# Optimization experiments

Measured on AMD Instinct MI355X. Metric: run time of the kernel, lower is better.

The kernel has to match this reference:

```python
import jax, jax.numpy as jnp
import numpy as np
import math

EMB_DIM = 1024
N_HEADS = 16
HEAD_DIM = EMB_DIM // N_HEADS
B, T = 4, 2048


def bitlinear(x, w):
    # BitNet b1.58 absmean ternary quantization. NOTE: the source never
    # rescales the ternary weights by `scale`, so forward uses raw {-1,0,1}.
    scale = jnp.maximum(jnp.mean(jnp.abs(w)), 1e-8)
    w_ternary = jnp.clip(jnp.round(w / scale), -1.0, 1.0)
    w_q = w + jax.lax.stop_gradient(w_ternary - w)  # STE
    return x @ w_q.T


def setup_inputs() -> dict:
    key = jax.random.key(0)
    k1, k2, k3 = jax.random.split(key, 3)
    x = jax.random.normal(k1, (B, T, EMB_DIM), dtype=jnp.float32)
    w_qkv = jax.random.normal(k2, (3 * EMB_DIM, EMB_DIM), dtype=jnp.float32) * 0.02
    w_out = jax.random.normal(k3, (EMB_DIM, EMB_DIM), dtype=jnp.float32) * 0.02
    return {"x": x, "w_qkv": w_qkv, "w_out": w_out}


def reference(x, w_qkv, w_out):
    Bc, Tc, C = x.shape
    qkv = bitlinear(x, w_qkv)  # [B, T, 3C]
    q, k, v = jnp.split(qkv, 3, axis=2)

    def split_heads(t):  # [B, T, C] -> [B, H, T, D]
        return t.reshape(Bc, Tc, N_HEADS, HEAD_DIM).transpose(0, 2, 1, 3)

    q, k, v = split_heads(q), split_heads(k), split_heads(v)
    scale = math.sqrt(HEAD_DIM)
    scores = jnp.einsum("bhqd,bhkd->bhqk", q, k) / scale  # [B, H, T, T]
    causal = jnp.triu(jnp.ones((Tc, Tc), dtype=bool), k=1)
    scores = jnp.where(causal, -jnp.inf, scores)
    attn = jax.nn.softmax(scores, axis=-1)
    out = jnp.einsum("bhqk,bhkd->bhqd", attn, v)  # [B, H, T, D]
    out = out.transpose(0, 2, 1, 3).reshape(Bc, Tc, C)
    return bitlinear(out, w_out)
```

## Files before the change

kernel.cpp:

```cpp
#include <hip/hip_runtime.h>
#include <hip/hip_bf16.h>

#define EMB   1024
#define NHEAD 16
#define HDIM  64
#define BSZ   4
#define SEQ   2048
#define MROWS (BSZ*SEQ)
#define NQKV  (3*EMB)

typedef __bf16 bf16;
typedef __bf16 bf16v4 __attribute__((ext_vector_type(4)));
typedef __bf16 bf16v8 __attribute__((ext_vector_type(8)));
typedef float  f32v4  __attribute__((ext_vector_type(4)));
typedef float  f32v16 __attribute__((ext_vector_type(16)));
typedef int    i32v4  __attribute__((ext_vector_type(4)));
typedef int    i32v16 __attribute__((ext_vector_type(16)));

#define MFMA16(a,b,c)   __builtin_amdgcn_mfma_f32_16x16x32_bf16((a),(b),(c),0,0,0)
#define MFMA32B(a,b,c)  __builtin_amdgcn_mfma_f32_32x32x16_bf16((a),(b),(c),0,0,0)
#define MFMAI8_32(a,b,c) __builtin_amdgcn_mfma_i32_32x32x32_i8((a),(b),(c),0,0,0)

__device__ __forceinline__ void gload_lds16(const void* g, void* l) {
  __builtin_amdgcn_global_load_lds((const __attribute__((address_space(1))) void*)g,
                                   (__attribute__((address_space(3))) void*)l,
                                   16, 0, 0);
}

#define DPP_FMAX(x, ctrl) do {                                                     \
    int _t = __builtin_amdgcn_update_dpp(0, __float_as_int(x), (ctrl), 0xf, 0xf, true); \
    (x) = fmaxf((x), __int_as_float(_t)); } while (0)


__global__ void abs_sum_kernel(const float* __restrict__ w, int n, float* out) {
  float s = 0.f;
  for (int i = blockIdx.x * blockDim.x + threadIdx.x; i < n; i += gridDim.x * blockDim.x)
    s += fabsf(w[i]);
  #pragma unroll
  for (int off = 32; off; off >>= 1) s += __shfl_down(s, off, 64);
  __shared__ float red[4];
  int lane = threadIdx.x & 63, wid = threadIdx.x >> 6;
  if (lane == 0) red[wid] = s;
  __syncthreads();
  if (threadIdx.x == 0) atomicAdd(out, red[0] + red[1] + red[2] + red[3]);
}

__global__ void ternarize_both_kernel(const float* __restrict__ wqkv,
                                      const float* __restrict__ wout,
                                      const float* __restrict__ sums,
                                      char* __restrict__ out8,
                                      bf16* __restrict__ outb) {
  int i = blockIdx.x * blockDim.x + threadIdx.x;
  const int N1 = NQKV * EMB;
  if (i < N1) {
    float scale = fmaxf(sums[0] / (float)N1, 1e-8f);
    float t = rintf(wqkv[i] / scale);
    out8[i] = (char)(int)fmaxf(-1.f, fminf(1.f, t));
  } else {
    int j = i - N1;
    float scale = fmaxf(sums[1] / (float)(EMB * EMB), 1e-8f);
    float t = rintf(wout[j] / scale);
    outb[j] = (bf16)fmaxf(-1.f, fminf(1.f, t));
  }
}

__global__ void quant_x_kernel(const float* __restrict__ x, char* __restrict__ p1,
                               char* __restrict__ p2, int n) {
  int i = blockIdx.x * blockDim.x + threadIdx.x;
  if (i >= n) return;
  float v = x[i];
  float q1 = fminf(fmaxf(rintf(v * 16.f), -127.f), 127.f);
  float r = v - q1 * 0.0625f;
  float q2 = fminf(fmaxf(rintf(r * 4096.f), -127.f), 127.f);
  p1[i] = (char)(int)q1;
  p2[i] = (char)(int)q2;
}


__launch_bounds__(256, 2)
__global__ void gemm_qkv_kernel(const char* __restrict__ xq1, const char* __restrict__ xq2,
                                const char* __restrict__ w8,
                                bf16* __restrict__ qh, bf16* __restrict__ ql,
                                bf16* __restrict__ kh, bf16* __restrict__ kl,
                                bf16* __restrict__ vt) {
  __shared__ __align__(16) char A1[3][128 * 64];
  __shared__ __align__(16) char A2[3][128 * 64];
  __shared__ __align__(16) char Bs[3][128 * 64];
  const int tid = threadIdx.x;
  const int lane = tid & 63, wid = tid >> 6;
  const int c31 = lane & 31, half = lane >> 5;
  const int m0 = blockIdx.x * 128, n0 = blockIdx.y * 128;
  const int wm = (wid >> 1) * 64, wn = (wid & 1) * 64;
  i32v16 acc1[2][2] = {};
  i32v16 acc2[2][2] = {};

  auto stage = [&](int bi, int kt) {
    #pragma unroll
    for (int r = 0; r < 2; ++r) {
      int li = r * 256 + tid;
      int row = li >> 2, cs = li & 3;
      int cg = cs ^ ((row >> 1) & 3);
      gload_lds16(xq1 + (size_t)(m0 + row) * EMB + kt * 64 + cg * 16, &A1[bi][li * 16]);
      gload_lds16(xq2 + (size_t)(m0 + row) * EMB + kt * 64 + cg * 16, &A2[bi][li * 16]);
      gload_lds16(w8  + (size_t)(n0 + row) * EMB + kt * 64 + cg * 16, &Bs[bi][li * 16]);
    }
  };

  stage(0, 0);
  for (int kt = 0; kt < EMB / 64; ++kt) {
    const int bi = kt % 3;
    if (kt + 1 < EMB / 64) {
      stage((kt + 1) % 3, kt + 1);
      asm volatile("s_waitcnt vmcnt(6)" ::: "memory");
    } else {
      asm volatile("s_waitcnt vmcnt(0)" ::: "memory");
    }
    __builtin_amdgcn_s_barrier();
    i32v4 a1[2][2], a2[2][2], bq[2][2];
    #pragma unroll
    for (int ks = 0; ks < 2; ++ks)
      #pragma unroll
      for (int tt = 0; tt < 2; ++tt) {
        int arow = wm + tt * 32 + c31;
        int aslot = (ks * 2 + half) ^ ((arow >> 1) & 3);
        a1[ks][tt] = *(const i32v4*)&A1[bi][arow * 64 + aslot * 16];
        a2[ks][tt] = *(const i32v4*)&A2[bi][arow * 64 + aslot * 16];
        int brow = wn + tt * 32 + c31;
        int bslot = (ks * 2 + half) ^ ((brow >> 1) & 3);
        bq[ks][tt] = *(const i32v4*)&Bs[bi][brow * 64 + bslot * 16];
      }
    #pragma unroll
    for (int ks = 0; ks < 2; ++ks)
      #pragma unroll
      for (int ti = 0; ti < 2; ++ti)
        #pragma unroll
        for (int tj = 0; tj < 2; ++tj) {
          acc1[ti][tj] = MFMAI8_32(a1[ks][ti], bq[ks][tj], acc1[ti][tj]);
          acc2[ti][tj] = MFMAI8_32(a2[ks][ti], bq[ks][tj], acc2[ti][tj]);
        }
  }
  const float S1 = 0.0625f, S2 = 1.f / 4096.f;
  const float QSCALE = 0.18033688011112042f;
  #pragma unroll
  for (int ti = 0; ti < 2; ++ti)
    #pragma unroll
    for (int tj = 0; tj < 2; ++tj) {
      const int n = n0 + wn + tj * 32 + c31;
      const int region = n >> 10, c1 = n & 1023, h = c1 >> 6, d = c1 & 63;
      #pragma unroll
      for (int g = 0; g < 4; ++g) {
        const int m_b = m0 + wm + ti * 32 + 8 * g + 4 * half;
        float c[4];
        #pragma unroll
        for (int rr = 0; rr < 4; ++rr)
          c[rr] = (float)acc1[ti][tj][g * 4 + rr] * S1 + (float)acc2[ti][tj][g * 4 + rr] * S2;
        if (region == 0) {
          #pragma unroll
          for (int rr = 0; rr < 4; ++rr) {
            int m = m_b + rr;
            int b = m >> 11, t = m & (SEQ - 1);
            size_t idx = (((size_t)(b * NHEAD + h) * SEQ + t) << 6) + d;
            float cs = c[rr] * QSCALE;
            bf16 hi = (bf16)cs;
            qh[idx] = hi; ql[idx] = (bf16)(cs - (float)hi);
          }
        } else if (region == 1) {
          #pragma unroll
          for (int rr = 0; rr < 4; ++rr) {
            int m = m_b + rr;
            int b = m >> 11, t = m & (SEQ - 1);
            size_t idx = (((size_t)(b * NHEAD + h) * SEQ + t) << 6) + d;
            bf16 hi = (bf16)c[rr];
            kh[idx] = hi; kl[idx] = (bf16)(c[rr] - (float)hi);
          }
        } else {
          bf16v4 pk;
          #pragma unroll
          for (int rr = 0; rr < 4; ++rr) pk[rr] = (bf16)c[rr];
          int b = m_b >> 11, t = m_b & (SEQ - 1);
          *(bf16v4*)&vt[((size_t)(b * NHEAD + h) * HDIM + d) * SEQ + t] = pk;
        }
      }
    }
}


__launch_bounds__(256, 2)
__global__ void attn_kernel(const bf16* __restrict__ qh, const bf16* __restrict__ ql,
                            const bf16* __restrict__ kh, const bf16* __restrict__ kl,
                            const bf16* __restrict__ vt, bf16* __restrict__ o) {
  __shared__ __align__(16) char smem[66560];
  bf16* Qh = (bf16*)smem;
  bf16* Ql = (bf16*)(smem + 16384);
  bf16* Pw = (bf16*)(smem + 49152);
  const int tid = threadIdx.x;
  const int lane = tid & 63, wid = tid >> 6;
  const int quad = lane >> 4, l16 = lane & 15;
  const int xs = l16 & 7;
  const int pair = blockIdx.x;
  const int bh = blockIdx.y;
  const size_t base = (size_t)bh * SEQ * HDIM;

  auto stage_kv = [&](char* dst, int k0) {
    #pragma unroll
    for (int r = 0; r < 2; ++r) {
      int li = r * 256 + tid;
      int srow = li >> 3, scg = (li & 7) ^ (srow & 7);
      gload_lds16(kh + base + (size_t)(k0 + srow) * HDIM + scg * 8, (bf16*)dst + (size_t)li * 8);
      gload_lds16(kl + base + (size_t)(k0 + srow) * HDIM + scg * 8, (bf16*)(dst + 8192) + (size_t)li * 8);
      gload_lds16(vt + base + (size_t)srow * SEQ + k0 + scg * 8,    (bf16*)(dst + 16384) + (size_t)li * 8);
    }
  };

  bf16v8 ones_f;
  {
    bf16 v1 = (l16 == 0) ? (bf16)1.0f : (bf16)0.0f;
    #pragma unroll
    for (int j = 0; j < 8; ++j) ones_f[j] = v1;
  }
  const int b = bh >> 4, h = bh & 15;

  for (int phase = 0; phase < 2; ++phase) {
    const int qt = phase ? (7 - pair) : (8 + pair);
    const int q0 = qt * 128;

    __syncthreads();
    #pragma unroll
    for (int r = 0; r < 4; ++r) {
      int li = r * 256 + tid;
      int row = li >> 3, cg = (li & 7) ^ (row & 7);
      gload_lds16(qh + base + (size_t)(q0 + row) * HDIM + cg * 8, &Qh[li * 8]);
      gload_lds16(ql + base + (size_t)(q0 + row) * HDIM + cg * 8, &Ql[li * 8]);
    }
    __syncthreads();
    bf16v8 qhf[2][2], qlf[2][2];
    #pragma unroll
    for (int sub = 0; sub < 2; ++sub)
      #pragma unroll
      for (int kk = 0; kk < 2; ++kk) {
        int off = (wid * 32 + sub * 16 + l16) * 64 + (((kk << 2) | quad) ^ xs) * 8;
        qhf[sub][kk] = *(const bf16v8*)&Qh[off];
        qlf[sub][kk] = *(const bf16v8*)&Ql[off];
      }
    __syncthreads();

    f32v4 oacc[2][4] = {};
    f32v4 lacc[2] = {};
    float mrow[2][4];
    #pragma unroll
    for (int s = 0; s < 2; ++s)
      #pragma unroll
      for (int r = 0; r < 4; ++r) mrow[s][r] = -1e30f;

    const int qw0 = q0 + wid * 32;
    const int qrow_hi = qw0 + 31;
    const int ntiles = 2 * qt + 2;

    stage_kv(smem, 0);

    for (int ktile = 0; ktile < ntiles; ++ktile) {
      char* cb = smem + (size_t)((ktile & 1) * 24576);
      char* nb = smem + (size_t)(((ktile + 1) & 1) * 24576);
      __syncthreads();
      if (ktile + 1 < ntiles) stage_kv(nb, (ktile + 1) * 64);
      const int k0 = ktile * 64;
      if (k0 > qrow_hi) continue;

      bf16* Kh_ = (bf16*)cb;
      bf16* Kl_ = (bf16*)(cb + 8192);
      bf16* Vt_ = (bf16*)(cb + 16384);

      f32v4 sacc[2][4] = {};
      #pragma unroll
      for (int kk = 0; kk < 2; ++kk) {
        const int co = (((kk << 2) | quad) ^ xs) * 8;
        bf16v8 khf[4], klf[4];
        #pragma unroll
        for (int nt = 0; nt < 4; ++nt) {
          khf[nt] = *(const bf16v8*)&Kh_[(nt * 16 + l16) * 64 + co];
          klf[nt] = *(const bf16v8*)&Kl_[(nt * 16 + l16) * 64 + co];
        }
        #pragma unroll
        for (int sub = 0; sub < 2; ++sub)
          #pragma unroll
          for (int nt = 0; nt < 4; ++nt) {
            sacc[sub][nt] = MFMA16(qhf[sub][kk], khf[nt], sacc[sub][nt]);
            sacc[sub][nt] = MFMA16(qhf[sub][kk], klf[nt], sacc[sub][nt]);
            sacc[sub][nt] = MFMA16(qlf[sub][kk], khf[nt], sacc[sub][nt]);
          }
      }

      #pragma unroll
      for (int sub = 0; sub < 2; ++sub) {
        if (k0 > qw0 + sub * 16 + 15) continue;
        const int qrow_base = qw0 + sub * 16 + quad * 4;
        #pragma unroll
        for (int nt = 0; nt < 4; ++nt) {
          int key = k0 + nt * 16 + l16;
          #pragma unroll
          for (int r = 0; r < 4; ++r)
            if (key > qrow_base + r) sacc[sub][nt][r] = -1e30f;
        }
        float alpha[4];
        #pragma unroll
        for (int r = 0; r < 4; ++r) {
          float mx = fmaxf(fmaxf(sacc[sub][0][r], sacc[sub][1][r]),
                           fmaxf(sacc[sub][2][r], sacc[sub][3][r]));
          DPP_FMAX(mx, 0x128);
          DPP_FMAX(mx, 0x124);
          DPP_FMAX(mx, 0x122);
          DPP_FMAX(mx, 0x121);
          float mnew = fmaxf(mrow[sub][r], mx);
          alpha[r] = __builtin_amdgcn_exp2f(mrow[sub][r] - mnew);
          mrow[sub][r] = mnew;
        }
        bf16* pwave = Pw + (wid * 2 + sub) * (16 * 68);
        #pragma unroll
        for (int nt = 0; nt < 4; ++nt)
          #pragma unroll
          for (int r = 0; r < 4; ++r)
            pwave[(quad * 4 + r) * 68 + nt * 16 + l16] =
                (bf16)__builtin_amdgcn_exp2f(sacc[sub][nt][r] - mrow[sub][r]);
        #pragma unroll
        for (int r = 0; r < 4; ++r) {
          lacc[sub][r] *= alpha[r];
          #pragma unroll
          for (int dt = 0; dt < 4; ++dt) oacc[sub][dt][r] *= alpha[r];
        }
      }

      #pragma unroll
      for (int kk = 0; kk < 2; ++kk) {
        const int co = (((kk << 2) | quad) ^ xs) * 8;
        bf16v8 vf[4];
        #pragma unroll
        for (int dt = 0; dt < 4; ++dt)
          vf[dt] = *(const bf16v8*)&Vt_[(dt * 16 + l16) * 64 + co];
        #pragma unroll
        for (int sub = 0; sub < 2; ++sub) {
          if (k0 > qw0 + sub * 16 + 15) continue;
          bf16v8 pf = *(const bf16v8*)&Pw[(wid * 2 + sub) * (16 * 68) + l16 * 68 + kk * 32 + quad * 8];
          lacc[sub] = MFMA16(pf, ones_f, lacc[sub]);
          #pragma unroll
          for (int dt = 0; dt < 4; ++dt)
            oacc[sub][dt] = MFMA16(pf, vf[dt], oacc[sub][dt]);
        }
      }
    }

    #pragma unroll
    for (int sub = 0; sub < 2; ++sub) {
      float lrow[4];
      #pragma unroll
      for (int r = 0; r < 4; ++r) lrow[r] = __shfl(lacc[sub][r], lane & 48, 64);
      #pragma unroll
      for (int dt = 0; dt < 4; ++dt)
        #pragma unroll
        for (int r = 0; r < 4; ++r) {
          int q = q0 + wid * 32 + sub * 16 + quad * 4 + r;
          int d = dt * 16 + l16;
          float val = oacc[sub][dt][r] / lrow[r];
          o[((size_t)(b * SEQ + q)) * EMB + h * HDIM + d] = (bf16)val;
        }
    }
  }
}


__launch_bounds__(256, 2)
__global__ void gemm_out_kernel(const bf16* __restrict__ oin, const bf16* __restrict__ wt,
                                float* __restrict__ out) {
  __shared__ __align__(16) bf16 As_[128 * 64];
  __shared__ __align__(16) bf16 Bs_[128 * 64];
  const int tid = threadIdx.x;
  const int lane = tid & 63, wid = tid >> 6;
  const int c31 = lane & 31, half = lane >> 5;
  const int m0 = blockIdx.x * 128, n0 = blockIdx.y * 128;
  const int wm = (wid >> 1) * 64, wn = (wid & 1) * 64;
  f32v16 acc[2][2] = {};

  for (int kt = 0; kt < EMB / 64; ++kt) {
    __syncthreads();
    #pragma unroll
    for (int r = 0; r < 4; ++r) {
      int li = r * 256 + tid;
      int row = li >> 3, cs = li & 7;
      int cg = cs ^ (row & 7);
      gload_lds16(oin + (size_t)(m0 + row) * EMB + kt * 64 + cg * 8, &As_[li * 8]);
      gload_lds16(wt  + (size_t)(n0 + row) * EMB + kt * 64 + cg * 8, &Bs_[li * 8]);
    }
    __syncthreads();
    bf16v8 af[4][2], bq[4][2];
    #pragma unroll
    for (int ks = 0; ks < 4; ++ks)
      #pragma unroll
      for (int tt = 0; tt < 2; ++tt) {
        int arow = wm + tt * 32 + c31;
        int aslot = (2 * ks + half) ^ (arow & 7);
        af[ks][tt] = *(const bf16v8*)&As_[arow * 64 + aslot * 8];
        int brow = wn + tt * 32 + c31;
        int bslot = (2 * ks + half) ^ (brow & 7);
        bq[ks][tt] = *(const bf16v8*)&Bs_[brow * 64 + bslot * 8];
      }
    #pragma unroll
    for (int ks = 0; ks < 4; ++ks)
      #pragma unroll
      for (int ti = 0; ti < 2; ++ti)
        #pragma unroll
        for (int tj = 0; tj < 2; ++tj)
          acc[ti][tj] = MFMA32B(af[ks][ti], bq[ks][tj], acc[ti][tj]);
  }
  #pragma unroll
  for (int ti = 0; ti < 2; ++ti)
    #pragma unroll
    for (int tj = 0; tj < 2; ++tj) {
      const int n = n0 + wn + tj * 32 + c31;
      #pragma unroll
      for (int g = 0; g < 4; ++g) {
        const int m_b = m0 + wm + ti * 32 + 8 * g + 4 * half;
        #pragma unroll
        for (int rr = 0; rr < 4; ++rr)
          out[(size_t)(m_b + rr) * EMB + n] = acc[ti][tj][g * 4 + rr];
      }
    }
}


extern "C" void kernel_launch(void* const* d_in, const int* in_sizes, int n_in,
                              void* d_out, int out_size, void* d_ws, size_t ws_size,
                              hipStream_t stream) {
  const float* x     = (const float*)d_in[0];
  const float* w_qkv = (const float*)d_in[1];
  const float* w_out = (const float*)d_in[2];
  float* out = (float*)d_out;
  char* ws = (char*)d_ws;

  const size_t SZ  = (size_t)MROWS * EMB * sizeof(bf16);
  const size_t SZ8 = (size_t)MROWS * EMB;
  size_t off = 0;
  float* sums = (float*)ws;            off = 256;
  char*  wq8  = (char*)(ws + off);     off += (size_t)NQKV * EMB;
  bf16*  wo_t = (bf16*)(ws + off);     off += (size_t)EMB * EMB * sizeof(bf16);
  char*  xq1  = (char*)(ws + off);     off += SZ8;
  char*  xq2  = (char*)(ws + off);     off += SZ8;
  bf16*  qh   = (bf16*)(ws + off);     off += SZ;
  bf16*  ql   = (bf16*)(ws + off);     off += SZ;
  bf16*  kh   = (bf16*)(ws + off);     off += SZ;
  bf16*  kl   = (bf16*)(ws + off);     off += SZ;
  bf16*  vt   = (bf16*)(ws + off);     off += SZ;
  bf16*  ob   = (bf16*)xq1;
  (void)in_sizes; (void)n_in; (void)out_size; (void)ws_size;

  hipMemsetAsync(sums, 0, 2 * sizeof(float), stream);
  abs_sum_kernel<<<256, 256, 0, stream>>>(w_qkv, NQKV * EMB, &sums[0]);
  abs_sum_kernel<<<256, 256, 0, stream>>>(w_out, EMB * EMB, &sums[1]);
  ternarize_both_kernel<<<(NQKV * EMB + EMB * EMB) / 256, 256, 0, stream>>>(w_qkv, w_out, sums, wq8, wo_t);
  quant_x_kernel<<<(MROWS * EMB) / 256, 256, 0, stream>>>(x, xq1, xq2, MROWS * EMB);
  gemm_qkv_kernel<<<dim3(MROWS / 128, NQKV / 128), 256, 0, stream>>>(xq1, xq2, wq8, qh, ql, kh, kl, vt);
  attn_kernel<<<dim3(8, BSZ * NHEAD), 256, 0, stream>>>(qh, ql, kh, kl, vt, ob);
  gemm_out_kernel<<<dim3(MROWS / 128, EMB / 128), 256, 0, stream>>>(ob, wo_t, out);
}
```

Measured before the change: 326.9 us.

## Vectorize prep kernels, add MFMA priority hints, multi-buffer output GEMM

The abs-sum, ternarize and activation-quantize kernels now load float4 and store 4-wide vectors, which cuts instruction count and memory transactions in these bandwidth-bound passes. The attention kernel wraps its MFMA sections in s_setprio so matrix work is issued ahead of other waves. The output GEMM moves from a single-buffered 64-wide K tile with two barriers per step to a 4-slot ring of 32-wide tiles, prefetching two tiles ahead with explicit vmcnt waits and one barrier per step, so global loads overlap compute. The hand-counted vmcnt values and the new swizzle must match exactly, or the GEMM reads stale or wrong data.

```diff
diff --git a/kernel.cpp b/kernel.cpp
--- a/kernel.cpp
+++ b/kernel.cpp
@@ -16,6 +16,7 @@
 typedef float  f32v16 __attribute__((ext_vector_type(16)));
 typedef int    i32v4  __attribute__((ext_vector_type(4)));
 typedef int    i32v16 __attribute__((ext_vector_type(16)));
+typedef char   c8v4   __attribute__((ext_vector_type(4)));
 
 #define MFMA16(a,b,c)   __builtin_amdgcn_mfma_f32_16x16x32_bf16((a),(b),(c),0,0,0)
 #define MFMA32B(a,b,c)  __builtin_amdgcn_mfma_f32_32x32x16_bf16((a),(b),(c),0,0,0)
@@ -32,10 +33,12 @@
     (x) = fmaxf((x), __int_as_float(_t)); } while (0)
 
 
-__global__ void abs_sum_kernel(const float* __restrict__ w, int n, float* out) {
+__global__ void abs_sum_kernel(const float4* __restrict__ w, int n4, float* out) {
   float s = 0.f;
-  for (int i = blockIdx.x * blockDim.x + threadIdx.x; i < n; i += gridDim.x * blockDim.x)
-    s += fabsf(w[i]);
+  for (int i = blockIdx.x * blockDim.x + threadIdx.x; i < n4; i += gridDim.x * blockDim.x) {
+    float4 v = w[i];
+    s += fabsf(v.x) + fabsf(v.y) + fabsf(v.z) + fabsf(v.w);
+  }
   #pragma unroll
   for (int off = 32; off; off >>= 1) s += __shfl_down(s, off, 64);
   __shared__ float red[4];
@@ -45,35 +48,52 @@
   if (threadIdx.x == 0) atomicAdd(out, red[0] + red[1] + red[2] + red[3]);
 }
 
-__global__ void ternarize_both_kernel(const float* __restrict__ wqkv,
-                                      const float* __restrict__ wout,
+__global__ void ternarize_both_kernel(const float4* __restrict__ wqkv,
+                                      const float4* __restrict__ wout,
                                       const float* __restrict__ sums,
-                                      char* __restrict__ out8,
-                                      bf16* __restrict__ outb) {
+                                      c8v4* __restrict__ out8,
+                                      bf16v4* __restrict__ outb) {
   int i = blockIdx.x * blockDim.x + threadIdx.x;
-  const int N1 = NQKV * EMB;
-  if (i < N1) {
-    float scale = fmaxf(sums[0] / (float)N1, 1e-8f);
-    float t = rintf(wqkv[i] / scale);
-    out8[i] = (char)(int)fmaxf(-1.f, fminf(1.f, t));
+  const int N1_4 = (NQKV * EMB) / 4;
+  if (i < N1_4) {
+    float scale = fmaxf(sums[0] / (float)(NQKV * EMB), 1e-8f);
+    float4 v = wqkv[i];
+    c8v4 o;
+    o[0] = (char)(int)fmaxf(-1.f, fminf(1.f, rintf(v.x / scale)));
+    o[1] = (char)(int)fmaxf(-1.f, fminf(1.f, rintf(v.y / scale)));
+    o[2] = (char)(int)fmaxf(-1.f, fminf(1.f, rintf(v.z / scale)));
+    o[3] = (char)(int)fmaxf(-1.f, fminf(1.f, rintf(v.w / scale)));
+    out8[i] = o;
   } else {
-    int j = i - N1;
+    int j = i - N1_4;
     float scale = fmaxf(sums[1] / (float)(EMB * EMB), 1e-8f);
-    float t = rintf(wout[j] / scale);
-    outb[j] = (bf16)fmaxf(-1.f, fminf(1.f, t));
-  }
-}
-
-__global__ void quant_x_kernel(const float* __restrict__ x, char* __restrict__ p1,
-                               char* __restrict__ p2, int n) {
+    float4 v = wout[j];
+    bf16v4 o;
+    o[0] = (bf16)fmaxf(-1.f, fminf(1.f, rintf(v.x / scale)));
+    o[1] = (bf16)fmaxf(-1.f, fminf(1.f, rintf(v.y / scale)));
+    o[2] = (bf16)fmaxf(-1.f, fminf(1.f, rintf(v.z / scale)));
+    o[3] = (bf16)fmaxf(-1.f, fminf(1.f, rintf(v.w / scale)));
+    outb[j] = o;
+  }
+}
+
+__global__ void quant_x_kernel(const float4* __restrict__ x, c8v4* __restrict__ p1,
+                               c8v4* __restrict__ p2, int n4) {
   int i = blockIdx.x * blockDim.x + threadIdx.x;
-  if (i >= n) return;
-  float v = x[i];
-  float q1 = fminf(fmaxf(rintf(v * 16.f), -127.f), 127.f);
-  float r = v - q1 * 0.0625f;
-  float q2 = fminf(fmaxf(rintf(r * 4096.f), -127.f), 127.f);
-  p1[i] = (char)(int)q1;
-  p2[i] = (char)(int)q2;
+  if (i >= n4) return;
+  float4 v = x[i];
+  c8v4 a, b;
+  float vv[4] = {v.x, v.y, v.z, v.w};
+  #pragma unroll
+  for (int k = 0; k < 4; ++k) {
+    float q1 = fminf(fmaxf(rintf(vv[k] * 16.f), -127.f), 127.f);
+    float r = vv[k] - q1 * 0.0625f;
+    float q2 = fminf(fmaxf(rintf(r * 4096.f), -127.f), 127.f);
+    a[k] = (char)(int)q1;
+    b[k] = (char)(int)q2;
+  }
+  p1[i] = a;
+  p2[i] = b;
 }
 
 
@@ -271,6 +291,7 @@
       bf16* Vt_ = (bf16*)(cb + 16384);
 
       f32v4 sacc[2][4] = {};
+      __builtin_amdgcn_s_setprio(1);
       #pragma unroll
       for (int kk = 0; kk < 2; ++kk) {
         const int co = (((kk << 2) | quad) ^ xs) * 8;
@@ -289,6 +310,7 @@
             sacc[sub][nt] = MFMA16(qlf[sub][kk], khf[nt], sacc[sub][nt]);
           }
       }
+      __builtin_amdgcn_s_setprio(0);
 
       #pragma unroll
       for (int sub = 0; sub < 2; ++sub) {
@@ -329,6 +351,7 @@
         }
       }
 
+      __builtin_amdgcn_s_setprio(1);
       #pragma unroll
       for (int kk = 0; kk < 2; ++kk) {
         const int co = (((kk << 2) | quad) ^ xs) * 8;
@@ -346,6 +369,7 @@
             oacc[sub][dt] = MFMA16(pf, vf[dt], oacc[sub][dt]);
         }
       }
+      __builtin_amdgcn_s_setprio(0);
     }
 
     #pragma unroll
@@ -370,40 +394,54 @@
 __launch_bounds__(256, 2)
 __global__ void gemm_out_kernel(const bf16* __restrict__ oin, const bf16* __restrict__ wt,
                                 float* __restrict__ out) {
-  __shared__ __align__(16) bf16 As_[128 * 64];
-  __shared__ __align__(16) bf16 Bs_[128 * 64];
+  __shared__ __align__(16) bf16 As_[4][128 * 32];
+  __shared__ __align__(16) bf16 Bs_[4][128 * 32];
   const int tid = threadIdx.x;
   const int lane = tid & 63, wid = tid >> 6;
   const int c31 = lane & 31, half = lane >> 5;
   const int m0 = blockIdx.x * 128, n0 = blockIdx.y * 128;
   const int wm = (wid >> 1) * 64, wn = (wid & 1) * 64;
   f32v16 acc[2][2] = {};
-
-  for (int kt = 0; kt < EMB / 64; ++kt) {
-    __syncthreads();
-    #pragma unroll
-    for (int r = 0; r < 4; ++r) {
+  const int NT = EMB / 32;
+
+  auto stage = [&](int bi, int kt) {
+    #pragma unroll
+    for (int r = 0; r < 2; ++r) {
       int li = r * 256 + tid;
-      int row = li >> 3, cs = li & 7;
-      int cg = cs ^ (row & 7);
-      gload_lds16(oin + (size_t)(m0 + row) * EMB + kt * 64 + cg * 8, &As_[li * 8]);
-      gload_lds16(wt  + (size_t)(n0 + row) * EMB + kt * 64 + cg * 8, &Bs_[li * 8]);
-    }
-    __syncthreads();
-    bf16v8 af[4][2], bq[4][2];
-    #pragma unroll
-    for (int ks = 0; ks < 4; ++ks)
+      int row = li >> 2, cs = li & 3;
+      int cg = cs ^ ((row >> 1) & 3);
+      gload_lds16(oin + (size_t)(m0 + row) * EMB + kt * 32 + cg * 8, &As_[bi][li * 8]);
+      gload_lds16(wt  + (size_t)(n0 + row) * EMB + kt * 32 + cg * 8, &Bs_[bi][li * 8]);
+    }
+  };
+
+  stage(0, 0);
+  stage(1, 1);
+  for (int kt = 0; kt < NT; ++kt) {
+    const int bi = kt & 3;
+    if (kt + 2 < NT) {
+      stage((kt + 2) & 3, kt + 2);
+      asm volatile("s_waitcnt vmcnt(8)" ::: "memory");
+    } else if (kt + 1 < NT) {
+      asm volatile("s_waitcnt vmcnt(4)" ::: "memory");
+    } else {
+      asm volatile("s_waitcnt vmcnt(0)" ::: "memory");
+    }
+    __builtin_amdgcn_s_barrier();
+    bf16v8 af[2][2], bq[2][2];
+    #pragma unroll
+    for (int ks = 0; ks < 2; ++ks)
       #pragma unroll
       for (int tt = 0; tt < 2; ++tt) {
         int arow = wm + tt * 32 + c31;
-        int aslot = (2 * ks + half) ^ (arow & 7);
-        af[ks][tt] = *(const bf16v8*)&As_[arow * 64 + aslot * 8];
+        int aslot = (2 * ks + half) ^ ((arow >> 1) & 3);
+        af[ks][tt] = *(const bf16v8*)&As_[bi][arow * 32 + aslot * 8];
         int brow = wn + tt * 32 + c31;
-        int bslot = (2 * ks + half) ^ (brow & 7);
-        bq[ks][tt] = *(const bf16v8*)&Bs_[brow * 64 + bslot * 8];
-      }
-    #pragma unroll
-    for (int ks = 0; ks < 4; ++ks)
+        int bslot = (2 * ks + half) ^ ((brow >> 1) & 3);
+        bq[ks][tt] = *(const bf16v8*)&Bs_[bi][brow * 32 + bslot * 8];
+      }
+    #pragma unroll
+    for (int ks = 0; ks < 2; ++ks)
       #pragma unroll
       for (int ti = 0; ti < 2; ++ti)
         #pragma unroll
@@ -452,10 +490,12 @@
   (void)in_sizes; (void)n_in; (void)out_size; (void)ws_size;
 
   hipMemsetAsync(sums, 0, 2 * sizeof(float), stream);
-  abs_sum_kernel<<<256, 256, 0, stream>>>(w_qkv, NQKV * EMB, &sums[0]);
-  abs_sum_kernel<<<256, 256, 0, stream>>>(w_out, EMB * EMB, &sums[1]);
-  ternarize_both_kernel<<<(NQKV * EMB + EMB * EMB) / 256, 256, 0, stream>>>(w_qkv, w_out, sums, wq8, wo_t);
-  quant_x_kernel<<<(MROWS * EMB) / 256, 256, 0, stream>>>(x, xq1, xq2, MROWS * EMB);
+  abs_sum_kernel<<<256, 256, 0, stream>>>((const float4*)w_qkv, (NQKV * EMB) / 4, &sums[0]);
+  abs_sum_kernel<<<256, 256, 0, stream>>>((const float4*)w_out, (EMB * EMB) / 4, &sums[1]);
+  ternarize_both_kernel<<<(NQKV * EMB + EMB * EMB) / 1024, 256, 0, stream>>>(
+      (const float4*)w_qkv, (const float4*)w_out, sums, (c8v4*)wq8, (bf16v4*)wo_t);
+  quant_x_kernel<<<(MROWS * EMB) / 1024, 256, 0, stream>>>(
+      (const float4*)x, (c8v4*)xq1, (c8v4*)xq2, (MROWS * EMB) / 4);
   gemm_qkv_kernel<<<dim3(MROWS / 128, NQKV / 128), 256, 0, stream>>>(xq1, xq2, wq8, qh, ql, kh, kl, vt);
   attn_kernel<<<dim3(8, BSZ * NHEAD), 256, 0, stream>>>(qh, ql, kh, kl, vt, ob);
   gemm_out_kernel<<<dim3(MROWS / 128, EMB / 128), 256, 0, stream>>>(ob, wo_t, out);
```

After: 315.5 us. 1.04x faster.
